# Kernel optimization log

Hardware: AMD Instinct MI355X
Metric: run time of the kernel (lower is better)

Reference implementation:

```python
import jax, jax.numpy as jnp
import numpy as np

NSX, NSY = 8, 8          # subdomain grid
BATCH = 8                # PDE instances
PTS = 100_000            # points per instance
IN_C, HID, OUT_C = 32, 64, 32
NUM_CLUSTERS = BATCH * NSX * NSY  # 512


def _clusters(coords, batch_ids):
    # coords assumed in [0,1]^2; bucket into NSX x NSY grid per batch sample
    ix = jnp.clip((coords[:, 0] * NSX).astype(jnp.int32), 0, NSX - 1)
    iy = jnp.clip((coords[:, 1] * NSY).astype(jnp.int32), 0, NSY - 1)
    return batch_ids * (NSX * NSY) + iy * NSX + ix


def _mlp(h, W1, b1, W2, b2):
    # Linear -> GELU(exact, matches torch nn.GELU default) -> Linear
    return jax.nn.gelu(h @ W1 + b1, approximate=False) @ W2 + b2


def setup_inputs() -> dict:
    key = jax.random.key(0)
    ks = jax.random.split(key, 12)
    N = BATCH * PTS
    x = jax.random.normal(ks[0], (N, IN_C), dtype=jnp.float32)
    src_coords = jax.random.uniform(ks[1], (N, 2), dtype=jnp.float32)
    tgt_coords = jax.random.uniform(ks[2], (N, 2), dtype=jnp.float32)
    src_batch = jnp.repeat(jnp.arange(BATCH, dtype=jnp.int32), PTS)
    tgt_batch = jnp.repeat(jnp.arange(BATCH, dtype=jnp.int32), PTS)
    def lin(k, fan_in, fan_out):
        s = 1.0 / np.sqrt(fan_in)
        kw, kb = jax.random.split(k)
        W = jax.random.uniform(kw, (fan_in, fan_out), minval=-s, maxval=s, dtype=jnp.float32)
        b = jax.random.uniform(kb, (fan_out,), minval=-s, maxval=s, dtype=jnp.float32)
        return W, b
    Wv1, bv1 = lin(ks[3], IN_C, HID)
    Wv2, bv2 = lin(ks[4], HID, HID)
    Wt1, bt1 = lin(ks[5], 2 + HID, HID)
    Wt2, bt2 = lin(ks[6], HID, OUT_C)
    return {"x": x, "src_coords": src_coords, "src_batch": src_batch,
            "tgt_coords": tgt_coords, "tgt_batch": tgt_batch,
            "Wv1": Wv1, "bv1": bv1, "Wv2": Wv2, "bv2": bv2,
            "Wt1": Wt1, "bt1": bt1, "Wt2": Wt2, "bt2": bt2}


def reference(x, src_coords, src_batch, tgt_coords, tgt_batch,
              Wv1, bv1, Wv2, bv2, Wt1, bt1, Wt2, bt2):
    src_cl = _clusters(src_coords, src_batch)        # [Ns]
    tgt_cl = _clusters(tgt_coords, tgt_batch)        # [Nt]
    h = _mlp(x, Wv1, bv1, Wv2, bv2)                  # [Ns, HID]
    # subdomain mean-pool (the integral over each subdomain)
    s = jax.ops.segment_sum(h, src_cl, num_segments=NUM_CLUSTERS)        # [C, HID]
    cnt = jax.ops.segment_sum(jnp.ones((h.shape[0], 1), h.dtype), src_cl,
                              num_segments=NUM_CLUSTERS)                 # [C, 1]
    pooled = s / jnp.maximum(cnt, 1.0)
    # broadcast pooled feature to each target point, concat target coords
    feat = jnp.concatenate([tgt_coords, pooled[tgt_cl]], axis=-1)        # [Nt, 2+HID]
    return _mlp(feat, Wt1, bt1, Wt2, bt2)            # [Nt, OUT_C]
```

## Files before the change

kernel.cpp:

```cpp
#include <hip/hip_runtime.h>

#define NC   512
#define INC  32
#define HID  64
#define OUTC 32
#define STRZ 68
#define GSTR 36

typedef __attribute__((ext_vector_type(8))) __bf16 bf16x8;
typedef __attribute__((ext_vector_type(4))) float  f32x4;
typedef __attribute__((ext_vector_type(8))) float  f32x8;
typedef __attribute__((ext_vector_type(8))) unsigned int   u32x8;
typedef __attribute__((ext_vector_type(8))) unsigned short u16x8;
typedef __attribute__((ext_vector_type(4))) unsigned short u16x4;

static __device__ __forceinline__ f32x4 mfma16(bf16x8 a, bf16x8 b, f32x4 c){
    return __builtin_amdgcn_mfma_f32_16x16x32_bf16(a, b, c, 0, 0, 0);
}

__device__ __forceinline__ float gelu_f(float v){
    const float s  = v * 0.70710678118654752f;
    const float as = fabsf(s);
    const float t  = __builtin_amdgcn_rcpf(__builtin_fmaf(0.3275911f, as, 1.0f));
    const float e  = __expf(-as * as);
    float p = __builtin_fmaf(1.061405429f, t, -1.453152027f);
    p = __builtin_fmaf(p, t, 1.421413741f);
    p = __builtin_fmaf(p, t, -0.284496736f);
    p = __builtin_fmaf(p, t, 0.254829592f);
    p = p * t;
    float er = __builtin_fmaf(-p, e, 1.0f);
    er = copysignf(er, s);
    return 0.5f * v * (1.0f + er);
}

__device__ __forceinline__ void split8v(f32x8 x, bf16x8& hi, bf16x8& lo){
    u32x8 ux = __builtin_bit_cast(u32x8, x);
    f32x8 hf = __builtin_bit_cast(f32x8, ux & 0xFFFF0000u);
    f32x8 lf = x - hf;
    u32x8 ul = __builtin_bit_cast(u32x8, lf);
    hi = __builtin_bit_cast(bf16x8, __builtin_convertvector(ux >> 16, u16x8));
    lo = __builtin_bit_cast(bf16x8, __builtin_convertvector(ul >> 16, u16x8));
}

__device__ __forceinline__ unsigned short rneb(float f){
    unsigned int u = __float_as_uint(f);
    u += 0x7FFFu + ((u >> 16) & 1u);
    return (unsigned short)(u >> 16);
}

__global__ __launch_bounds__(256, 3) void k_src(
    const float* __restrict__ x, const float* __restrict__ sc,
    const float* __restrict__ Wv1, const float* __restrict__ bv1,
    float* __restrict__ partial, float* __restrict__ pcntf,
    int npb, int T, int bpb)
{
    __shared__ ushort gbuf[2][4][64][GSTR];
    __shared__ ushort lcw[2][4][32];
    const int t = threadIdx.x;
    const int wave = t >> 6, lane = t & 63;
    const int lrow = lane & 15, lgrp = lane >> 4;
    const int batch = blockIdx.x / bpb;
    const int pb    = blockIdx.x % bpb;

    bf16x8 Bh0, Bh1, Bh2, Bh3, Bl0, Bl1, Bl2, Bl3;
    float bnt0, bnt1, bnt2, bnt3;
    {
        f32x8 w;
        #pragma unroll
        for (int j = 0; j < 8; j++) w[j] = Wv1[(8*lgrp + j)*HID +  0 + lrow];
        split8v(w, Bh0, Bl0);  bnt0 = bv1[ 0 + lrow];
        #pragma unroll
        for (int j = 0; j < 8; j++) w[j] = Wv1[(8*lgrp + j)*HID + 16 + lrow];
        split8v(w, Bh1, Bl1);  bnt1 = bv1[16 + lrow];
        #pragma unroll
        for (int j = 0; j < 8; j++) w[j] = Wv1[(8*lgrp + j)*HID + 32 + lrow];
        split8v(w, Bh2, Bl2);  bnt2 = bv1[32 + lrow];
        #pragma unroll
        for (int j = 0; j < 8; j++) w[j] = Wv1[(8*lgrp + j)*HID + 48 + lrow];
        split8v(w, Bh3, Bl3);  bnt3 = bv1[48 + lrow];
    }
    u16x8 onesu;
    #pragma unroll
    for (int j = 0; j < 8; j++) onesu[j] = 0x3F80u;
    const bf16x8 ONE = __builtin_bit_cast(bf16x8, onesu);

    f32x4 P0 = (f32x4){0.f,0.f,0.f,0.f}, P1 = P0, P2 = P0, P3 = P0, C = P0;

    const int base   = batch * npb + pb * T * 16;
    const int PAIRS  = T >> 1;
    const int rounds = (PAIRS + 3) >> 2;

    int  p_cur  = wave;
    bool a_cur  = p_cur < PAIRS;
    float2 sA_c, sB_c; f32x8 xA_c, xB_c;
    if (a_cur){
        const int pt0 = base + p_cur * 32;
        sA_c = ((const float2*)sc)[pt0 + lrow];
        sB_c = ((const float2*)sc)[pt0 + 16 + lrow];
        xA_c = *(const f32x8*)(x + (size_t)(pt0 + lrow)*INC + 8*lgrp);
        xB_c = *(const f32x8*)(x + (size_t)(pt0 + 16 + lrow)*INC + 8*lgrp);
    }

    for (int r = 0; r < rounds; r++){
        const int buf = r & 1;
        const int  p_nxt = p_cur + 4;
        const bool a_nxt = p_nxt < PAIRS;
        float2 sA_n, sB_n; f32x8 xA_n, xB_n;
        if (a_nxt){
            const int pt0 = base + p_nxt * 32;
            sA_n = ((const float2*)sc)[pt0 + lrow];
            sB_n = ((const float2*)sc)[pt0 + 16 + lrow];
            xA_n = *(const f32x8*)(x + (size_t)(pt0 + lrow)*INC + 8*lgrp);
            xB_n = *(const f32x8*)(x + (size_t)(pt0 + 16 + lrow)*INC + 8*lgrp);
        }

        if (a_cur){
            int ixA = (int)(sA_c.x * 8.0f); ixA = ixA < 0 ? 0 : (ixA > 7 ? 7 : ixA);
            int iyA = (int)(sA_c.y * 8.0f); iyA = iyA < 0 ? 0 : (iyA > 7 ? 7 : iyA);
            int ixB = (int)(sB_c.x * 8.0f); ixB = ixB < 0 ? 0 : (ixB > 7 ? 7 : ixB);
            int iyB = (int)(sB_c.y * 8.0f); iyB = iyB < 0 ? 0 : (iyB > 7 ? 7 : iyB);
            if (lgrp == 0){
                lcw[buf][wave][lrow]      = (ushort)((iyA << 3) + ixA);
                lcw[buf][wave][16 + lrow] = (ushort)((iyB << 3) + ixB);
            }
            {
                bf16x8 Ah, Al; split8v(xA_c, Ah, Al);
                f32x4 a0 = (f32x4){0.f,0.f,0.f,0.f}, a1 = a0, a2 = a0, a3 = a0;
                a0 = mfma16(Al, Bh0, a0); a1 = mfma16(Al, Bh1, a1);
                a2 = mfma16(Al, Bh2, a2); a3 = mfma16(Al, Bh3, a3);
                a0 = mfma16(Ah, Bl0, a0); a1 = mfma16(Ah, Bl1, a1);
                a2 = mfma16(Ah, Bl2, a2); a3 = mfma16(Ah, Bl3, a3);
                a0 = mfma16(Ah, Bh0, a0); a1 = mfma16(Ah, Bh1, a1);
                a2 = mfma16(Ah, Bh2, a2); a3 = mfma16(Ah, Bh3, a3);
                u16x4 w4;
                w4[0]=rneb(gelu_f(a0[0]+bnt0)); w4[1]=rneb(gelu_f(a0[1]+bnt0));
                w4[2]=rneb(gelu_f(a0[2]+bnt0)); w4[3]=rneb(gelu_f(a0[3]+bnt0));
                *(u16x4*)&gbuf[buf][wave][ 0 + lrow][4*lgrp] = w4;
                w4[0]=rneb(gelu_f(a1[0]+bnt1)); w4[1]=rneb(gelu_f(a1[1]+bnt1));
                w4[2]=rneb(gelu_f(a1[2]+bnt1)); w4[3]=rneb(gelu_f(a1[3]+bnt1));
                *(u16x4*)&gbuf[buf][wave][16 + lrow][4*lgrp] = w4;
                w4[0]=rneb(gelu_f(a2[0]+bnt2)); w4[1]=rneb(gelu_f(a2[1]+bnt2));
                w4[2]=rneb(gelu_f(a2[2]+bnt2)); w4[3]=rneb(gelu_f(a2[3]+bnt2));
                *(u16x4*)&gbuf[buf][wave][32 + lrow][4*lgrp] = w4;
                w4[0]=rneb(gelu_f(a3[0]+bnt3)); w4[1]=rneb(gelu_f(a3[1]+bnt3));
                w4[2]=rneb(gelu_f(a3[2]+bnt3)); w4[3]=rneb(gelu_f(a3[3]+bnt3));
                *(u16x4*)&gbuf[buf][wave][48 + lrow][4*lgrp] = w4;
            }
            {
                bf16x8 Ah, Al; split8v(xB_c, Ah, Al);
                f32x4 a0 = (f32x4){0.f,0.f,0.f,0.f}, a1 = a0, a2 = a0, a3 = a0;
                a0 = mfma16(Al, Bh0, a0); a1 = mfma16(Al, Bh1, a1);
                a2 = mfma16(Al, Bh2, a2); a3 = mfma16(Al, Bh3, a3);
                a0 = mfma16(Ah, Bl0, a0); a1 = mfma16(Ah, Bl1, a1);
                a2 = mfma16(Ah, Bl2, a2); a3 = mfma16(Ah, Bl3, a3);
                a0 = mfma16(Ah, Bh0, a0); a1 = mfma16(Ah, Bh1, a1);
                a2 = mfma16(Ah, Bh2, a2); a3 = mfma16(Ah, Bh3, a3);
                u16x4 w4;
                w4[0]=rneb(gelu_f(a0[0]+bnt0)); w4[1]=rneb(gelu_f(a0[1]+bnt0));
                w4[2]=rneb(gelu_f(a0[2]+bnt0)); w4[3]=rneb(gelu_f(a0[3]+bnt0));
                *(u16x4*)&gbuf[buf][wave][ 0 + lrow][16 + 4*lgrp] = w4;
                w4[0]=rneb(gelu_f(a1[0]+bnt1)); w4[1]=rneb(gelu_f(a1[1]+bnt1));
                w4[2]=rneb(gelu_f(a1[2]+bnt1)); w4[3]=rneb(gelu_f(a1[3]+bnt1));
                *(u16x4*)&gbuf[buf][wave][16 + lrow][16 + 4*lgrp] = w4;
                w4[0]=rneb(gelu_f(a2[0]+bnt2)); w4[1]=rneb(gelu_f(a2[1]+bnt2));
                w4[2]=rneb(gelu_f(a2[2]+bnt2)); w4[3]=rneb(gelu_f(a2[3]+bnt2));
                *(u16x4*)&gbuf[buf][wave][32 + lrow][16 + 4*lgrp] = w4;
                w4[0]=rneb(gelu_f(a3[0]+bnt3)); w4[1]=rneb(gelu_f(a3[1]+bnt3));
                w4[2]=rneb(gelu_f(a3[2]+bnt3)); w4[3]=rneb(gelu_f(a3[3]+bnt3));
                *(u16x4*)&gbuf[buf][wave][48 + lrow][16 + 4*lgrp] = w4;
            }
        } else {
            if (lgrp == 0){
                lcw[buf][wave][lrow]      = 0xFFFFu;
                lcw[buf][wave][16 + lrow] = 0xFFFFu;
            }
            u16x4 zz = (u16x4){0,0,0,0};
            #pragma unroll
            for (int nt = 0; nt < 4; nt++){
                *(u16x4*)&gbuf[buf][wave][16*nt + lrow][4*lgrp] = zz;
                *(u16x4*)&gbuf[buf][wave][16*nt + lrow][16 + 4*lgrp] = zz;
            }
        }
        __syncthreads();

        const ushort tgt = (ushort)(16*wave + lrow);
        #pragma unroll
        for (int s = 0; s < 4; s++){
            const u16x8 lcv = *(const u16x8*)&lcw[buf][s][8*lgrp];
            u16x8 ohu;
            #pragma unroll
            for (int j = 0; j < 8; j++)
                ohu[j] = (lcv[j] == tgt) ? (ushort)0x3F80u : (ushort)0;
            const bf16x8 oh = __builtin_bit_cast(bf16x8, ohu);
            u16x4 glo, ghi;
            glo = *(const u16x4*)&gbuf[buf][s][ 0 + lrow][8*lgrp];
            ghi = *(const u16x4*)&gbuf[buf][s][ 0 + lrow][8*lgrp + 4];
            bf16x8 g0 = __builtin_bit_cast(bf16x8, __builtin_shufflevector(glo, ghi, 0,1,2,3,4,5,6,7));
            glo = *(const u16x4*)&gbuf[buf][s][16 + lrow][8*lgrp];
            ghi = *(const u16x4*)&gbuf[buf][s][16 + lrow][8*lgrp + 4];
            bf16x8 g1 = __builtin_bit_cast(bf16x8, __builtin_shufflevector(glo, ghi, 0,1,2,3,4,5,6,7));
            glo = *(const u16x4*)&gbuf[buf][s][32 + lrow][8*lgrp];
            ghi = *(const u16x4*)&gbuf[buf][s][32 + lrow][8*lgrp + 4];
            bf16x8 g2 = __builtin_bit_cast(bf16x8, __builtin_shufflevector(glo, ghi, 0,1,2,3,4,5,6,7));
            glo = *(const u16x4*)&gbuf[buf][s][48 + lrow][8*lgrp];
            ghi = *(const u16x4*)&gbuf[buf][s][48 + lrow][8*lgrp + 4];
            bf16x8 g3 = __builtin_bit_cast(bf16x8, __builtin_shufflevector(glo, ghi, 0,1,2,3,4,5,6,7));
            P0 = mfma16(oh, g0, P0);
            P1 = mfma16(oh, g1, P1);
            P2 = mfma16(oh, g2, P2);
            P3 = mfma16(oh, g3, P3);
            C  = mfma16(oh, ONE, C);
        }

        p_cur = p_nxt; a_cur = a_nxt;
        sA_c = sA_n; sB_c = sB_n; xA_c = xA_n; xB_c = xB_n;
    }

    float* dst = partial + (size_t)blockIdx.x * 4096;
    #pragma unroll
    for (int reg = 0; reg < 4; reg++){
        const int row = 16*wave + 4*lgrp + reg;
        dst[row*64 +  0 + lrow] = P0[reg];
        dst[row*64 + 16 + lrow] = P1[reg];
        dst[row*64 + 32 + lrow] = P2[reg];
        dst[row*64 + 48 + lrow] = P3[reg];
    }
    if (lrow == 0){
        #pragma unroll
        for (int reg = 0; reg < 4; reg++)
            pcntf[(size_t)blockIdx.x*64 + 16*wave + 4*lgrp + reg] = C[reg];
    }
}

__global__ __launch_bounds__(256) void k_cluster(
    const float* __restrict__ partial, const float* __restrict__ pcntf,
    const float* __restrict__ Wv2, const float* __restrict__ bv2,
    const float* __restrict__ Wt1, const float* __restrict__ bt1,
    float* __restrict__ z, int spb)
{
    __shared__ float red[4][HID];
    __shared__ float redn[4];
    __shared__ float m[HID];
    __shared__ float ph[HID];
    const int c = blockIdx.x;
    const int t = threadIdx.x, j = t & 63, sl = t >> 6;
    const int batch = c >> 6, lc = c & 63;

    float s = 0.0f, cn = 0.0f;
    for (int b = sl; b < spb; b += 4){
        const size_t slot = (size_t)batch * spb + b;
        s  += partial[slot * 4096 + (size_t)lc * 64 + j];
        cn += pcntf[slot * 64 + lc];
    }
    red[sl][j] = s;
    if (j == 0) redn[sl] = cn;
    __syncthreads();

    if (sl == 0){
        float stot = red[0][j] + red[1][j] + red[2][j] + red[3][j];
        float ntot = redn[0] + redn[1] + redn[2] + redn[3];
        const float inv = (ntot > 0.0f) ? (1.0f / ntot) : 0.0f;
        m[j] = stot * inv;
        __builtin_amdgcn_s_barrier();
        float a = bv2[j];
        #pragma unroll 8
        for (int i = 0; i < HID; i++) a += m[i] * Wv2[i*HID + j];
        if (ntot <= 0.0f) a = 0.0f;
        ph[j] = a;
        __builtin_amdgcn_s_barrier();
        float b = bt1[j];
        #pragma unroll 8
        for (int i = 0; i < HID; i++) b += ph[i] * Wt1[(2 + i)*HID + j];
        z[c*HID + j] = b;
    }
}

__global__ __launch_bounds__(256, 3) void k_tgt(
    const float* __restrict__ tc,
    const float* __restrict__ z, const float* __restrict__ Wt1,
    const float* __restrict__ Wt2, const float* __restrict__ bt2,
    float* __restrict__ out, int npb, int TT, int bpt)
{
    __shared__ float zs[64*STRZ];
    const int t = threadIdx.x;
    const int wave = t >> 6, lane = t & 63;
    const int lrow = lane & 15, lgrp = lane >> 4;
    const int batch = blockIdx.x / bpt;
    const int toff  = (blockIdx.x % bpt) * TT;

    for (int k = t; k < 4096; k += 256)
        zs[(k >> 6)*STRZ + (k & 63)] = z[(size_t)(batch*64)*HID + k];

    bf16x8 Bh00, Bh01, Bh10, Bh11, Bl00, Bl01, Bl10, Bl11;
    f32x8 w0v0, w0v1, w1v0, w1v1;
    {
        f32x8 w;
        #pragma unroll
        for (int j = 0; j < 8; j++) w[j] = Wt2[( 0 + 8*lgrp + j)*OUTC +  0 + lrow];
        split8v(w, Bh00, Bl00);
        #pragma unroll
        for (int j = 0; j < 8; j++) w[j] = Wt2[( 0 + 8*lgrp + j)*OUTC + 16 + lrow];
        split8v(w, Bh01, Bl01);
        #pragma unroll
        for (int j = 0; j < 8; j++) w[j] = Wt2[(32 + 8*lgrp + j)*OUTC +  0 + lrow];
        split8v(w, Bh10, Bl10);
        #pragma unroll
        for (int j = 0; j < 8; j++) w[j] = Wt2[(32 + 8*lgrp + j)*OUTC + 16 + lrow];
        split8v(w, Bh11, Bl11);
        #pragma unroll
        for (int j = 0; j < 8; j++){
            w0v0[j] = Wt1[ 0 + 8*lgrp + j];
            w0v1[j] = Wt1[32 + 8*lgrp + j];
            w1v0[j] = Wt1[HID +  0 + 8*lgrp + j];
            w1v1[j] = Wt1[HID + 32 + 8*lgrp + j];
        }
    }
    const float bo0 = bt2[lrow], bo1 = bt2[16 + lrow];
    __syncthreads();

    const size_t pbase = (size_t)batch * npb;
    float2 c2_c = ((const float2*)tc)[pbase + (size_t)(toff + wave)*16 + lrow];

    for (int tt = toff + wave; tt < toff + TT; tt += 4){
        const int ttn = tt + 4;
        float2 c2_n = c2_c;
        if (ttn < toff + TT)
            c2_n = ((const float2*)tc)[pbase + (size_t)ttn*16 + lrow];

        int ix = (int)(c2_c.x * 8.0f); ix = ix < 0 ? 0 : (ix > 7 ? 7 : ix);
        int iy = (int)(c2_c.y * 8.0f); iy = iy < 0 ? 0 : (iy > 7 ? 7 : iy);
        const int zb = ((iy << 3) + ix) * STRZ;

        f32x8 z0 = *(const f32x8*)(&zs[zb +  0 + 8*lgrp]);
        f32x8 z1 = *(const f32x8*)(&zs[zb + 32 + 8*lgrp]);
        f32x8 g0, g1;
        #pragma unroll
        for (int j = 0; j < 8; j++){
            g0[j] = gelu_f(z0[j] + c2_c.x * w0v0[j] + c2_c.y * w1v0[j]);
            g1[j] = gelu_f(z1[j] + c2_c.x * w0v1[j] + c2_c.y * w1v1[j]);
        }
        bf16x8 Ah0, Al0, Ah1, Al1;
        split8v(g0, Ah0, Al0);
        split8v(g1, Ah1, Al1);

        f32x4 a0 = (f32x4){0.f,0.f,0.f,0.f}, a1 = a0;
        a0 = mfma16(Al0, Bh00, a0); a1 = mfma16(Al0, Bh01, a1);
        a0 = mfma16(Ah0, Bl00, a0); a1 = mfma16(Ah0, Bl01, a1);
        a0 = mfma16(Ah0, Bh00, a0); a1 = mfma16(Ah0, Bh01, a1);
        a0 = mfma16(Al1, Bh10, a0); a1 = mfma16(Al1, Bh11, a1);
        a0 = mfma16(Ah1, Bl10, a0); a1 = mfma16(Ah1, Bl11, a1);
        a0 = mfma16(Ah1, Bh10, a0); a1 = mfma16(Ah1, Bh11, a1);

        const size_t prow = pbase + (size_t)tt*16 + 4*lgrp;
        #pragma unroll
        for (int q = 0; q < 4; q++){
            out[(prow + q)*OUTC +  0 + lrow] = a0[q] + bo0;
            out[(prow + q)*OUTC + 16 + lrow] = a1[q] + bo1;
        }
        c2_c = c2_n;
    }
}

extern "C" void kernel_launch(void* const* d_in, const int* in_sizes, int n_in,
                              void* d_out, int out_size, void* d_ws, size_t ws_size,
                              hipStream_t stream)
{
    const float* x   = (const float*)d_in[0];
    const float* sc  = (const float*)d_in[1];
    const int*   sb  = (const int*)  d_in[2];  (void)sb;
    const float* tc  = (const float*)d_in[3];
    const int*   tb  = (const int*)  d_in[4];  (void)tb;
    const float* Wv1 = (const float*)d_in[5];
    const float* bv1 = (const float*)d_in[6];
    const float* Wv2 = (const float*)d_in[7];
    const float* bv2 = (const float*)d_in[8];
    const float* Wt1 = (const float*)d_in[9];
    const float* bt1 = (const float*)d_in[10];
    const float* Wt2 = (const float*)d_in[11];
    const float* bt2 = (const float*)d_in[12];
    float* out = (float*)d_out;

    const int n   = in_sizes[2];
    const int npb = n / 8;
    const int tiles_pb = npb / 16;

    int bpb = 1;
    const int cands[4] = {125, 25, 5, 1};
    for (int ci = 0; ci < 4; ci++){
        const int d = cands[ci];
        if (tiles_pb % d) continue;
        if ((tiles_pb / d) & 1) continue;
        const size_t slots = (size_t)8 * d;
        const size_t need  = slots * 4096 * 4 + slots * 64 * 4 + (size_t)NC*HID*4 + 4096;
        if (need <= ws_size){ bpb = d; break; }
    }
    const int T    = tiles_pb / bpb;
    const int nblk = 8 * bpb;
    const size_t slots = (size_t)nblk;

    char* ws = (char*)d_ws;
    float* partial = (float*)(ws);
    float* pcntf   = (float*)(ws + slots * 4096 * 4);
    float* z       = (float*)(ws + slots * 4096 * 4 + slots * 64 * 4);

    k_src    <<<nblk, 256, 0, stream>>>(x, sc, Wv1, bv1, partial, pcntf, npb, T, bpb);
    k_cluster<<<NC, 256, 0, stream>>>(partial, pcntf, Wv2, bv2, Wt1, bt1, z, bpb);

    int TT = 1;
    const int tcands[5] = {25, 10, 5, 2, 1};
    for (int ci = 0; ci < 5; ci++){
        if (tiles_pb % tcands[ci] == 0){ TT = tcands[ci]; break; }
    }
    const int bpt = tiles_pb / TT;
    k_tgt    <<<8*bpt, 256, 0, stream>>>(tc, z, Wt1, Wt2, bt2, out, npb, TT, bpt);
}
```

Baseline: 108.2 us.

## Single-buffer source LDS staging, drop x low-part MFMA, raise occupancy to 4

```diff
diff --git a/kernel.cpp b/kernel.cpp
--- a/kernel.cpp
+++ b/kernel.cpp
@@ -48,14 +48,14 @@
     return (unsigned short)(u >> 16);
 }
 
-__global__ __launch_bounds__(256, 3) void k_src(
+__global__ __launch_bounds__(256, 4) void k_src(
     const float* __restrict__ x, const float* __restrict__ sc,
     const float* __restrict__ Wv1, const float* __restrict__ bv1,
     float* __restrict__ partial, float* __restrict__ pcntf,
     int npb, int T, int bpb)
 {
-    __shared__ ushort gbuf[2][4][64][GSTR];
-    __shared__ ushort lcw[2][4][32];
+    __shared__ ushort gbuf[4][64][GSTR];
+    __shared__ ushort lcw[4][32];
     const int t = threadIdx.x;
     const int wave = t >> 6, lane = t & 63;
     const int lrow = lane & 15, lgrp = lane >> 4;
@@ -102,7 +102,6 @@
     }
 
     for (int r = 0; r < rounds; r++){
-        const int buf = r & 1;
         const int  p_nxt = p_cur + 4;
         const bool a_nxt = p_nxt < PAIRS;
         float2 sA_n, sB_n; f32x8 xA_n, xB_n;
@@ -114,96 +113,90 @@
             xB_n = *(const f32x8*)(x + (size_t)(pt0 + 16 + lrow)*INC + 8*lgrp);
         }
 
+        int lcA = 0, lcB = 0;
+        u16x4 wA0, wA1, wA2, wA3, wB0, wB1, wB2, wB3;
         if (a_cur){
             int ixA = (int)(sA_c.x * 8.0f); ixA = ixA < 0 ? 0 : (ixA > 7 ? 7 : ixA);
             int iyA = (int)(sA_c.y * 8.0f); iyA = iyA < 0 ? 0 : (iyA > 7 ? 7 : iyA);
             int ixB = (int)(sB_c.x * 8.0f); ixB = ixB < 0 ? 0 : (ixB > 7 ? 7 : ixB);
             int iyB = (int)(sB_c.y * 8.0f); iyB = iyB < 0 ? 0 : (iyB > 7 ? 7 : iyB);
-            if (lgrp == 0){
-                lcw[buf][wave][lrow]      = (ushort)((iyA << 3) + ixA);
-                lcw[buf][wave][16 + lrow] = (ushort)((iyB << 3) + ixB);
-            }
+            lcA = (iyA << 3) + ixA;
+            lcB = (iyB << 3) + ixB;
             {
-                bf16x8 Ah, Al; split8v(xA_c, Ah, Al);
+                bf16x8 Ah = __builtin_convertvector(xA_c, bf16x8);
                 f32x4 a0 = (f32x4){0.f,0.f,0.f,0.f}, a1 = a0, a2 = a0, a3 = a0;
-                a0 = mfma16(Al, Bh0, a0); a1 = mfma16(Al, Bh1, a1);
-                a2 = mfma16(Al, Bh2, a2); a3 = mfma16(Al, Bh3, a3);
                 a0 = mfma16(Ah, Bl0, a0); a1 = mfma16(Ah, Bl1, a1);
                 a2 = mfma16(Ah, Bl2, a2); a3 = mfma16(Ah, Bl3, a3);
                 a0 = mfma16(Ah, Bh0, a0); a1 = mfma16(Ah, Bh1, a1);
                 a2 = mfma16(Ah, Bh2, a2); a3 = mfma16(Ah, Bh3, a3);
-                u16x4 w4;
-                w4[0]=rneb(gelu_f(a0[0]+bnt0)); w4[1]=rneb(gelu_f(a0[1]+bnt0));
-                w4[2]=rneb(gelu_f(a0[2]+bnt0)); w4[3]=rneb(gelu_f(a0[3]+bnt0));
-                *(u16x4*)&gbuf[buf][wave][ 0 + lrow][4*lgrp] = w4;
-                w4[0]=rneb(gelu_f(a1[0]+bnt1)); w4[1]=rneb(gelu_f(a1[1]+bnt1));
-                w4[2]=rneb(gelu_f(a1[2]+bnt1)); w4[3]=rneb(gelu_f(a1[3]+bnt1));
-                *(u16x4*)&gbuf[buf][wave][16 + lrow][4*lgrp] = w4;
-                w4[0]=rneb(gelu_f(a2[0]+bnt2)); w4[1]=rneb(gelu_f(a2[1]+bnt2));
-                w4[2]=rneb(gelu_f(a2[2]+bnt2)); w4[3]=rneb(gelu_f(a2[3]+bnt2));
-                *(u16x4*)&gbuf[buf][wave][32 + lrow][4*lgrp] = w4;
-                w4[0]=rneb(gelu_f(a3[0]+bnt3)); w4[1]=rneb(gelu_f(a3[1]+bnt3));
-                w4[2]=rneb(gelu_f(a3[2]+bnt3)); w4[3]=rneb(gelu_f(a3[3]+bnt3));
-                *(u16x4*)&gbuf[buf][wave][48 + lrow][4*lgrp] = w4;
+                wA0[0]=rneb(gelu_f(a0[0]+bnt0)); wA0[1]=rneb(gelu_f(a0[1]+bnt0));
+                wA0[2]=rneb(gelu_f(a0[2]+bnt0)); wA0[3]=rneb(gelu_f(a0[3]+bnt0));
+                wA1[0]=rneb(gelu_f(a1[0]+bnt1)); wA1[1]=rneb(gelu_f(a1[1]+bnt1));
+                wA1[2]=rneb(gelu_f(a1[2]+bnt1)); wA1[3]=rneb(gelu_f(a1[3]+bnt1));
+                wA2[0]=rneb(gelu_f(a2[0]+bnt2)); wA2[1]=rneb(gelu_f(a2[1]+bnt2));
+                wA2[2]=rneb(gelu_f(a2[2]+bnt2)); wA2[3]=rneb(gelu_f(a2[3]+bnt2));
+                wA3[0]=rneb(gelu_f(a3[0]+bnt3)); wA3[1]=rneb(gelu_f(a3[1]+bnt3));
+                wA3[2]=rneb(gelu_f(a3[2]+bnt3)); wA3[3]=rneb(gelu_f(a3[3]+bnt3));
             }
             {
-                bf16x8 Ah, Al; split8v(xB_c, Ah, Al);
+                bf16x8 Ah = __builtin_convertvector(xB_c, bf16x8);
                 f32x4 a0 = (f32x4){0.f,0.f,0.f,0.f}, a1 = a0, a2 = a0, a3 = a0;
-                a0 = mfma16(Al, Bh0, a0); a1 = mfma16(Al, Bh1, a1);
-                a2 = mfma16(Al, Bh2, a2); a3 = mfma16(Al, Bh3, a3);
                 a0 = mfma16(Ah, Bl0, a0); a1 = mfma16(Ah, Bl1, a1);
                 a2 = mfma16(Ah, Bl2, a2); a3 = mfma16(Ah, Bl3, a3);
                 a0 = mfma16(Ah, Bh0, a0); a1 = mfma16(Ah, Bh1, a1);
                 a2 = mfma16(Ah, Bh2, a2); a3 = mfma16(Ah, Bh3, a3);
-                u16x4 w4;
-                w4[0]=rneb(gelu_f(a0[0]+bnt0)); w4[1]=rneb(gelu_f(a0[1]+bnt0));
-                w4[2]=rneb(gelu_f(a0[2]+bnt0)); w4[3]=rneb(gelu_f(a0[3]+bnt0));
-                *(u16x4*)&gbuf[buf][wave][ 0 + lrow][16 + 4*lgrp] = w4;
-                w4[0]=rneb(gelu_f(a1[0]+bnt1)); w4[1]=rneb(gelu_f(a1[1]+bnt1));
-                w4[2]=rneb(gelu_f(a1[2]+bnt1)); w4[3]=rneb(gelu_f(a1[3]+bnt1));
-                *(u16x4*)&gbuf[buf][wave][16 + lrow][16 + 4*lgrp] = w4;
-                w4[0]=rneb(gelu_f(a2[0]+bnt2)); w4[1]=rneb(gelu_f(a2[1]+bnt2));
-                w4[2]=rneb(gelu_f(a2[2]+bnt2)); w4[3]=rneb(gelu_f(a2[3]+bnt2));
-                *(u16x4*)&gbuf[buf][wave][32 + lrow][16 + 4*lgrp] = w4;
-                w4[0]=rneb(gelu_f(a3[0]+bnt3)); w4[1]=rneb(gelu_f(a3[1]+bnt3));
-                w4[2]=rneb(gelu_f(a3[2]+bnt3)); w4[3]=rneb(gelu_f(a3[3]+bnt3));
-                *(u16x4*)&gbuf[buf][wave][48 + lrow][16 + 4*lgrp] = w4;
+                wB0[0]=rneb(gelu_f(a0[0]+bnt0)); wB0[1]=rneb(gelu_f(a0[1]+bnt0));
+                wB0[2]=rneb(gelu_f(a0[2]+bnt0)); wB0[3]=rneb(gelu_f(a0[3]+bnt0));
+                wB1[0]=rneb(gelu_f(a1[0]+bnt1)); wB1[1]=rneb(gelu_f(a1[1]+bnt1));
+                wB1[2]=rneb(gelu_f(a1[2]+bnt1)); wB1[3]=rneb(gelu_f(a1[3]+bnt1));
+                wB2[0]=rneb(gelu_f(a2[0]+bnt2)); wB2[1]=rneb(gelu_f(a2[1]+bnt2));
+                wB2[2]=rneb(gelu_f(a2[2]+bnt2)); wB2[3]=rneb(gelu_f(a2[3]+bnt2));
+                wB3[0]=rneb(gelu_f(a3[0]+bnt3)); wB3[1]=rneb(gelu_f(a3[1]+bnt3));
+                wB3[2]=rneb(gelu_f(a3[2]+bnt3)); wB3[3]=rneb(gelu_f(a3[3]+bnt3));
             }
         } else {
-            if (lgrp == 0){
-                lcw[buf][wave][lrow]      = 0xFFFFu;
-                lcw[buf][wave][16 + lrow] = 0xFFFFu;
-            }
-            u16x4 zz = (u16x4){0,0,0,0};
-            #pragma unroll
-            for (int nt = 0; nt < 4; nt++){
-                *(u16x4*)&gbuf[buf][wave][16*nt + lrow][4*lgrp] = zz;
-                *(u16x4*)&gbuf[buf][wave][16*nt + lrow][16 + 4*lgrp] = zz;
-            }
-        }
+            wA0 = (u16x4){0,0,0,0}; wA1 = wA0; wA2 = wA0; wA3 = wA0;
+            wB0 = wA0; wB1 = wA0; wB2 = wA0; wB3 = wA0;
+        }
+
         __syncthreads();
 
+        if (lgrp == 0){
+            lcw[wave][lrow]      = a_cur ? (ushort)lcA : (ushort)0xFFFFu;
+            lcw[wave][16 + lrow] = a_cur ? (ushort)lcB : (ushort)0xFFFFu;
+        }
+        *(u16x4*)&gbuf[wave][ 0 + lrow][4*lgrp] = wA0;
+        *(u16x4*)&gbuf[wave][16 + lrow][4*lgrp] = wA1;
+        *(u16x4*)&gbuf[wave][32 + lrow][4*lgrp] = wA2;
+        *(u16x4*)&gbuf[wave][48 + lrow][4*lgrp] = wA3;
+        *(u16x4*)&gbuf[wave][ 0 + lrow][16 + 4*lgrp] = wB0;
+        *(u16x4*)&gbuf[wave][16 + lrow][16 + 4*lgrp] = wB1;
+        *(u16x4*)&gbuf[wave][32 + lrow][16 + 4*lgrp] = wB2;
+        *(u16x4*)&gbuf[wave][48 + lrow][16 + 4*lgrp] = wB3;
+
+        __syncthreads();
+
         const ushort tgt = (ushort)(16*wave + lrow);
         #pragma unroll
         for (int s = 0; s < 4; s++){
-            const u16x8 lcv = *(const u16x8*)&lcw[buf][s][8*lgrp];
+            const u16x8 lcv = *(const u16x8*)&lcw[s][8*lgrp];
             u16x8 ohu;
             #pragma unroll
             for (int j = 0; j < 8; j++)
                 ohu[j] = (lcv[j] == tgt) ? (ushort)0x3F80u : (ushort)0;
             const bf16x8 oh = __builtin_bit_cast(bf16x8, ohu);
             u16x4 glo, ghi;
-            glo = *(const u16x4*)&gbuf[buf][s][ 0 + lrow][8*lgrp];
-            ghi = *(const u16x4*)&gbuf[buf][s][ 0 + lrow][8*lgrp + 4];
+            glo = *(const u16x4*)&gbuf[s][ 0 + lrow][8*lgrp];
+            ghi = *(const u16x4*)&gbuf[s][ 0 + lrow][8*lgrp + 4];
             bf16x8 g0 = __builtin_bit_cast(bf16x8, __builtin_shufflevector(glo, ghi, 0,1,2,3,4,5,6,7));
-            glo = *(const u16x4*)&gbuf[buf][s][16 + lrow][8*lgrp];
-            ghi = *(const u16x4*)&gbuf[buf][s][16 + lrow][8*lgrp + 4];
+            glo = *(const u16x4*)&gbuf[s][16 + lrow][8*lgrp];
+            ghi = *(const u16x4*)&gbuf[s][16 + lrow][8*lgrp + 4];
             bf16x8 g1 = __builtin_bit_cast(bf16x8, __builtin_shufflevector(glo, ghi, 0,1,2,3,4,5,6,7));
-            glo = *(const u16x4*)&gbuf[buf][s][32 + lrow][8*lgrp];
-            ghi = *(const u16x4*)&gbuf[buf][s][32 + lrow][8*lgrp + 4];
+            glo = *(const u16x4*)&gbuf[s][32 + lrow][8*lgrp];
+            ghi = *(const u16x4*)&gbuf[s][32 + lrow][8*lgrp + 4];
             bf16x8 g2 = __builtin_bit_cast(bf16x8, __builtin_shufflevector(glo, ghi, 0,1,2,3,4,5,6,7));
-            glo = *(const u16x4*)&gbuf[buf][s][48 + lrow][8*lgrp];
-            ghi = *(const u16x4*)&gbuf[buf][s][48 + lrow][8*lgrp + 4];
+            glo = *(const u16x4*)&gbuf[s][48 + lrow][8*lgrp];
+            ghi = *(const u16x4*)&gbuf[s][48 + lrow][8*lgrp + 4];
             bf16x8 g3 = __builtin_bit_cast(bf16x8, __builtin_shufflevector(glo, ghi, 0,1,2,3,4,5,6,7));
             P0 = mfma16(oh, g0, P0);
             P1 = mfma16(oh, g1, P1);
```

Measured after the change: 190.3 us. +75.9%, slower.
